# Performance work log

Hardware: AMD Instinct MI355X
Metric: run time of the kernel (lower is better)

The kernel has to match this reference:

```python
import jax, jax.numpy as jnp
import numpy as np

BN_EPS = 1e-5


def _bn(x, gamma, beta):
    # x: [B, C, L]; training-mode BatchNorm1d: biased stats over (B, L) per channel.
    mu = x.mean(axis=(0, 2), keepdims=True)
    var = x.var(axis=(0, 2), keepdims=True)
    return (x - mu) * jax.lax.rsqrt(var + BN_EPS) * gamma[None, :, None] + beta[None, :, None]


def _sblock(x, g1, be1, w1, bi1, g2, be2, w2, bi2):
    # x: [B, m, n] (n == m). bn1 over channel dim n after transpose.
    t = jnp.swapaxes(x, -2, -1)                      # [B, n, m]
    t = jax.nn.relu(_bn(t, g1, be1))
    t = jnp.einsum('bnm,km->bnk', t, w1) + bi1       # Linear(n,n) on last dim
    t = jnp.swapaxes(t, -2, -1)                      # [B, m, n]
    t = jax.nn.relu(_bn(t, g2, be2))                 # bn2 over channel dim m
    t = jnp.einsum('bmn,kn->bmk', t, w2) + bi2       # Linear(m,m) on last dim
    return t


def _forward(x, bn1_gamma, bn1_beta, w1, b1, bn2_gamma, bn2_beta, w2, b2):
    out = x
    num_blocks = w1.shape[0]
    for l in range(num_blocks):
        out = _sblock(out, bn1_gamma[l], bn1_beta[l], w1[l], b1[l],
                      bn2_gamma[l], bn2_beta[l], w2[l], b2[l])
    n, m = out.shape[-2], out.shape[-1]

    # greedy argmax row/col masking on a detached copy (batch index 0, as in torch)
    oc0 = jax.lax.stop_gradient(out[0])              # [n, m]
    neg_inf = jnp.float32(-jnp.inf)

    def body(line, state):
        oc, visited, mask = state
        idx = jnp.argmax(oc)
        i, j = idx // m, idx % m
        visited = visited.at[i].set(1.0)
        mask = mask.at[:, j].set(1.0 - visited)
        oc = oc.at[:, j].set(neg_inf)
        oc = oc.at[i, :].set(neg_inf)
        return oc, visited, mask

    init = (oc0, jnp.zeros((n,), jnp.float32), jnp.zeros((n, m), jnp.float32))
    _, _, mask = jax.lax.fori_loop(0, n, body, init)

    out = jnp.where(mask.astype(bool)[None], neg_inf, out)
    return jax.nn.softmax(out, axis=-1)


def setup_inputs() -> dict:
    key = jax.random.key(0)
    ks = jax.random.split(key, 9)
    L, n, m = 2, 2048, 2048
    return {
        'x': jax.random.normal(ks[0], (1, m, n), jnp.float32),
        'bn1_gamma': jax.random.uniform(ks[1], (L, n), jnp.float32, 0.5, 1.5),
        'bn1_beta': 0.1 * jax.random.normal(ks[2], (L, n), jnp.float32),
        'w1': 0.02 * jax.random.normal(ks[3], (L, n, n), jnp.float32),
        'b1': 0.02 * jax.random.normal(ks[4], (L, n), jnp.float32),
        'bn2_gamma': jax.random.uniform(ks[5], (L, m), jnp.float32, 0.5, 1.5),
        'bn2_beta': 0.1 * jax.random.normal(ks[6], (L, m), jnp.float32),
        'w2': 0.02 * jax.random.normal(ks[7], (L, m, m), jnp.float32),
        'b2': 0.02 * jax.random.normal(ks[8], (L, m), jnp.float32),
    }


def reference(x, bn1_gamma, bn1_beta, w1, b1, bn2_gamma, bn2_beta, w2, b2):
    return _forward(x, bn1_gamma, bn1_beta, w1, b1, bn2_gamma, bn2_beta, w2, b2)
```

## Files before the change

### kernel.cpp

```cpp
#include <hip/hip_runtime.h>
#include <math.h>

#define NEG_INF (-__builtin_inf())

typedef unsigned long long u64;

constexpr int N = 2048;
constexpr int NCHUNK = 32;
constexpr int RPC = N / NCHUNK;
constexpr int K_LIST = 64;
constexpr int BCAND = 128;
constexpr int CMAX = 256;
constexpr int CTGT = 240;
constexpr int POOL_MIN = 48;

template<typename T> struct Key;
template<> struct Key<float>{
  static __device__ inline u64 pack(float x){
    unsigned u = __float_as_uint(x);
    u = (u & 0x80000000u) ? ~u : (u | 0x80000000u);
    return ((u64)u) << 32;
  }
};

__device__ inline bool kbetter(u64 k, unsigned rc, u64 bk, unsigned brc){
  return (k > bk) || (k == bk && rc < brc);
}

template<typename T>
__global__ __launch_bounds__(256) void colstats_partial(const T* __restrict__ X, double* __restrict__ part){
  int col = blockIdx.x * 256 + threadIdx.x;
  int r0  = blockIdx.y * RPC;
  double s = 0.0, q = 0.0;
  for (int r = r0; r < r0 + RPC; ++r){
    double v = (double)X[(size_t)r * N + col];
    s += v; q += v * v;
  }
  size_t o = (size_t)blockIdx.y * N + col;
  part[o*2+0] = s; part[o*2+1] = q;
}

__global__ __launch_bounds__(256) void colstats_final(const double* __restrict__ part,
    const float* __restrict__ g, const float* __restrict__ be,
    double* __restrict__ A, double* __restrict__ C){
  int col = blockIdx.x * 256 + threadIdx.x;
  double s = 0.0, q = 0.0;
  for (int k = 0; k < NCHUNK; ++k){
    size_t o = (size_t)k * N + col;
    s += part[o*2+0]; q += part[o*2+1];
  }
  double mu  = s / (double)N;
  double var = q / (double)N - mu * mu;
  double inv = 1.0 / sqrt(var + 1e-5);
  double a = (double)g[col] * inv;
  A[col] = a;
  C[col] = (double)be[col] - mu * a;
}

template<typename T>
__global__ __launch_bounds__(256) void rowstats(const T* __restrict__ Z,
    const float* __restrict__ g, const float* __restrict__ be,
    double* __restrict__ A, double* __restrict__ C){
  __shared__ double s1[256], s2[256];
  int r = blockIdx.x, tx = threadIdx.x;
  double s = 0.0, q = 0.0;
  for (int j = tx; j < N; j += 256){
    double v = (double)Z[(size_t)r * N + j];
    s += v; q += v * v;
  }
  s1[tx] = s; s2[tx] = q; __syncthreads();
  for (int st = 128; st; st >>= 1){
    if (tx < st){ s1[tx] += s1[tx + st]; s2[tx] += s2[tx + st]; }
    __syncthreads();
  }
  if (tx == 0){
    double mu  = s1[0] / (double)N;
    double var = s2[0] / (double)N - mu * mu;
    double inv = 1.0 / sqrt(var + 1e-5);
    double a = (double)g[r] * inv;
    A[r] = a;
    C[r] = (double)be[r] - mu * a;
  }
}

template<typename Tin, typename Tout>
__global__ __launch_bounds__(256) void bnrelu_col(const Tin* __restrict__ X,
    const double* __restrict__ A, const double* __restrict__ C, Tout* __restrict__ O){
  int i = blockIdx.x;
  for (int j = threadIdx.x; j < N; j += 256){
    double v = fma((double)X[(size_t)i * N + j], A[j], C[j]);
    O[(size_t)i * N + j] = (Tout)(v > 0.0 ? v : 0.0);
  }
}

template<typename Tin, typename Tout>
__global__ __launch_bounds__(256) void bnrelu_row(const Tin* __restrict__ Z,
    const double* __restrict__ A, const double* __restrict__ C, Tout* __restrict__ O){
  int i = blockIdx.x;
  double a = A[i], c = C[i];
  for (int j = threadIdx.x; j < N; j += 256){
    double v = fma((double)Z[(size_t)i * N + j], a, c);
    O[(size_t)i * N + j] = (Tout)(v > 0.0 ? v : 0.0);
  }
}

template<typename TA, typename TB, typename TO, typename TACC, bool BT, bool BIAS_ROW>
__global__ __launch_bounds__(256) void gemm_t(const TA* __restrict__ A, const TB* __restrict__ B,
    const float* __restrict__ bias, TO* __restrict__ O){
  __shared__ TACC sA[16][68];
  __shared__ TACC sB[16][68];
  const int tid = threadIdx.x;
  const int tx = tid & 15, ty = tid >> 4;
  const int i0 = blockIdx.y * 64, j0 = blockIdx.x * 64;
  TACC acc[4][4] = {};
  for (int k0 = 0; k0 < N; k0 += 16){
    {
      int r = tid >> 2, c4 = (tid & 3) * 4;
      const TA* p = A + (size_t)(i0 + r) * N + k0 + c4;
      TACC v0 = (TACC)p[0], v1 = (TACC)p[1], v2 = (TACC)p[2], v3 = (TACC)p[3];
      sA[c4+0][r] = v0; sA[c4+1][r] = v1; sA[c4+2][r] = v2; sA[c4+3][r] = v3;
    }
    if (!BT){
      int k = tid >> 4, j4 = (tid & 15) * 4;
      const TB* p = B + (size_t)(k0 + k) * N + j0 + j4;
      sB[k][j4+0] = (TACC)p[0]; sB[k][j4+1] = (TACC)p[1];
      sB[k][j4+2] = (TACC)p[2]; sB[k][j4+3] = (TACC)p[3];
    } else {
      int j = tid >> 2, c4 = (tid & 3) * 4;
      const TB* p = B + (size_t)(j0 + j) * N + k0 + c4;
      TACC v0 = (TACC)p[0], v1 = (TACC)p[1], v2 = (TACC)p[2], v3 = (TACC)p[3];
      sB[c4+0][j] = v0; sB[c4+1][j] = v1; sB[c4+2][j] = v2; sB[c4+3][j] = v3;
    }
    __syncthreads();
    #pragma unroll
    for (int kk = 0; kk < 16; ++kk){
      TACC a_[4], b_[4];
      #pragma unroll
      for (int q = 0; q < 4; ++q){ a_[q] = sA[kk][ty*4+q]; b_[q] = sB[kk][tx*4+q]; }
      #pragma unroll
      for (int mi = 0; mi < 4; ++mi)
        #pragma unroll
        for (int ni = 0; ni < 4; ++ni)
          acc[mi][ni] = fma(a_[mi], b_[ni], acc[mi][ni]);
    }
    __syncthreads();
  }
  #pragma unroll
  for (int mi = 0; mi < 4; ++mi){
    int i = i0 + ty*4 + mi;
    #pragma unroll
    for (int ni = 0; ni < 4; ++ni){
      int j = j0 + tx*4 + ni;
      TACC bv = BIAS_ROW ? (TACC)bias[i] : (TACC)bias[j];
      O[(size_t)i * N + j] = (TO)(acc[mi][ni] + bv);
    }
  }
}

template<typename T>
__global__ __launch_bounds__(256) void build_lists(const T* __restrict__ O,
    ulonglong2* __restrict__ list, unsigned short* __restrict__ llen,
    u64* __restrict__ rvK_g, unsigned* __restrict__ rvRC_g,
    unsigned* __restrict__ flag){
  __shared__ unsigned hist4[4][256];
  __shared__ unsigned hsum[256];
  __shared__ u64 candK[BCAND];
  __shared__ unsigned candRC[BCAND];
  __shared__ u64 redK[256];
  __shared__ unsigned redC[256];
  __shared__ u64 sTau;
  __shared__ unsigned sBstar, sPre, sDone, sC;
  const int r = blockIdx.x;
  const int tid = threadIdx.x;
  const int wave = tid >> 6, lane = tid & 63;
  const unsigned BIG = 0xFFFFFFFFu;
  const T* __restrict__ row = O + (size_t)r * N;
  const unsigned target = K_LIST;

  if (r == 0 && tid == 0) *flag = 0u;

  u64 base = 0; unsigned pre = 0; int shift = 56;
  for (int level = 0; level < 8; ++level){
    for (int i = tid; i < 4*256; i += 256) ((unsigned*)hist4)[i] = 0;
    __syncthreads();
    for (int c = tid; c < N; c += 256){
      u64 k = Key<T>::pack(row[c]);
      if (k >= base && ((k - base) >> shift) < 256)
        atomicAdd(&hist4[wave][(unsigned)((k - base) >> shift)], 1u);
    }
    __syncthreads();
    if (tid < 256) hsum[tid] = hist4[0][tid] + hist4[1][tid] + hist4[2][tid] + hist4[3][tid];
    __syncthreads();
    if (wave == 0){
      unsigned v0 = hsum[4*lane+0], v1 = hsum[4*lane+1], v2 = hsum[4*lane+2], v3 = hsum[4*lane+3];
      unsigned s3 = v3, s2 = v2+v3, s1 = v1+s2, tot = v0+s1;
      unsigned run = tot;
      #pragma unroll
      for (int off = 1; off < 64; off <<= 1){
        unsigned x = __shfl_down(run, off);
        if (lane + off < 64) run += x;
      }
      unsigned above = run - tot;
      unsigned ge0 = tot + above, ge1 = s1 + above, ge2 = s2 + above, ge3 = s3 + above;
      int bl = -1; unsigned geb = 0, vb = 0;
      if (pre + ge3 >= target){ bl = 4*lane+3; geb = ge3; vb = v3; }
      else if (pre + ge2 >= target){ bl = 4*lane+2; geb = ge2; vb = v2; }
      else if (pre + ge1 >= target){ bl = 4*lane+1; geb = ge1; vb = v1; }
      else if (pre + ge0 >= target){ bl = 4*lane+0; geb = ge0; vb = v0; }
      int bmax = bl;
      #pragma unroll
      for (int off = 32; off; off >>= 1){
        int o = __shfl_xor(bmax, off);
        if (o > bmax) bmax = o;
      }
      if (bmax < 0){
        if (lane == 0){ sBstar = 0; sPre = pre; sDone = 1; }
      } else if (bl == bmax){
        unsigned total = pre + geb;
        sBstar = (unsigned)bmax; sPre = pre + geb - vb;
        sDone = (total <= BCAND || shift == 0) ? 1u : 0u;
      }
    }
    __syncthreads();
    unsigned bstar = sBstar;
    if (sDone){
      if (tid == 0) sTau = base + ((u64)bstar << shift);
      break;
    }
    base += ((u64)bstar << shift);
    pre = sPre;
    shift -= 8;
    __syncthreads();
  }
  __syncthreads();
  const u64 tau = sTau;

  if (tid == 0) sC = 0;
  __syncthreads();
  for (int c = tid; c < N; c += 256){
    u64 k = Key<T>::pack(row[c]);
    if (k >= tau){
      unsigned p = atomicAdd(&sC, 1u);
      if (p < BCAND){ candK[p] = k; candRC[p] = ((unsigned)r << 11) | (unsigned)c; }
    }
  }
  __syncthreads();
  unsigned C = sC;

  if (C > BCAND){
    u64 bk = 0; unsigned bc = BIG;
    for (int c = tid; c < N; c += 256){
      u64 k = Key<T>::pack(row[c]);
      if (k > bk){ bk = k; bc = (unsigned)c; }
    }
    redK[tid] = bk; redC[tid] = bc; __syncthreads();
    for (int st = 128; st; st >>= 1){
      if (tid < st && kbetter(redK[tid+st], redC[tid+st], redK[tid], redC[tid])){
        redK[tid] = redK[tid+st]; redC[tid] = redC[tid+st];
      }
      __syncthreads();
    }
    if (tid == 0){
      llen[r] = 0;
      rvK_g[r] = redK[0];
      rvRC_g[r] = ((unsigned)r << 11) | (redC[0] & 2047u);
    }
    return;
  }

  unsigned S = 64; while (S < C) S <<= 1;
  for (unsigned p = C + tid; p < S; p += 256){ candK[p] = 0; candRC[p] = BIG; }
  __syncthreads();
  for (unsigned k2 = 2; k2 <= S; k2 <<= 1){
    for (unsigned jj = k2 >> 1; jj > 0; jj >>= 1){
      if (tid < (int)(S >> 1)){
        unsigned i = (((unsigned)tid & ~(jj - 1)) << 1) | ((unsigned)tid & (jj - 1));
        unsigned l = i | jj;
        bool up = ((i & k2) == 0);
        u64 ki = candK[i], kl = candK[l];
        unsigned ri = candRC[i], rl = candRC[l];
        bool lBeforeI = (kl > ki) || (kl == ki && rl < ri);
        bool iBeforeL = (ki > kl) || (ki == kl && ri < rl);
        if (up ? lBeforeI : iBeforeL){
          candK[i] = kl; candK[l] = ki; candRC[i] = rl; candRC[l] = ri;
        }
      }
      __syncthreads();
    }
  }

  unsigned outLen = (C < (unsigned)K_LIST) ? C : (unsigned)K_LIST;
  if (tid < (int)outLen){
    ulonglong2 e; e.x = candK[tid]; e.y = (u64)candRC[tid];
    list[(size_t)r * K_LIST + tid] = e;
  }
  if (tid == 0){
    llen[r] = (unsigned short)outLen;
    rvK_g[r] = candK[0];
    rvRC_g[r] = candRC[0];
  }
}

template<typename T>
__global__ __launch_bounds__(512) void greedy9c(const T* __restrict__ O,
    const ulonglong2* __restrict__ list, const unsigned short* __restrict__ llen_g,
    const u64* __restrict__ rvK_g, const unsigned* __restrict__ rvRC_g,
    unsigned* __restrict__ rowStep_g, unsigned* __restrict__ colStep_g,
    unsigned* __restrict__ flag){
  __shared__ u64 rvK[N];
  __shared__ unsigned rvRC[N];
  __shared__ unsigned cm32[N/32];
  __shared__ unsigned short hIdx[N];
  __shared__ unsigned short hLen[N];
  __shared__ unsigned rowStepL[N];
  __shared__ unsigned colStepL[N];
  __shared__ unsigned hist[8][256];
  __shared__ unsigned hsum[256];
  __shared__ u64 candK[CMAX];
  __shared__ unsigned candRC[CMAX];
  __shared__ u64 sortK[CMAX];
  __shared__ unsigned sortRC[CMAX];
  __shared__ unsigned foc[N];
  __shared__ u64 redK8[8];
  __shared__ unsigned redC8[8];
  __shared__ u64 sTau, sTauP;
  __shared__ unsigned sBstar, sPre, sDone, sC, sCnt, sL, sPC;
  const int tid  = threadIdx.x;
  const int lane = tid & 63, wave = tid >> 6;
  const unsigned BIG = 0xFFFFFFFFu;
  const u64 lmask = ((u64)1 << lane) - 1;

  if (blockIdx.x != 0){
    __shared__ unsigned sdone;
    float a = 1.0f;
    const float b = 1.0000001f, c = 1e-7f;
    for (;;){
      if (tid == 0) sdone = atomicAdd(flag, 0u);
      __syncthreads();
      unsigned d = sdone;
      __syncthreads();
      if (d) break;
      #pragma unroll 8
      for (int i = 0; i < 512; ++i) a = fmaf(a, b, c);
      asm volatile("" : "+v"(a));
    }
    return;
  }

  for (int i = tid; i < N; i += 512){
    rvK[i] = rvK_g[i]; rvRC[i] = rvRC_g[i];
    unsigned short L0 = llen_g[i];
    hLen[i] = L0;
    hIdx[i] = (L0 == 0) ? (unsigned short)0xFFFFu : (unsigned short)1;
  }
  if (tid < N/32) cm32[tid] = 0xFFFFFFFFu;
  if (tid == 0){ sPC = 0; sTauP = 0; sCnt = 0; sL = BIG; }
  __syncthreads();

  unsigned t = 0;
  for (int rd = 0; rd < N && t < N; ++rd){
    const unsigned alive = N - t;
    const unsigned PCin = sPC;
    const bool needRadix = (PCin < (unsigned)POOL_MIN) && (PCin < alive);

    unsigned PC;
    u64 tau;
    bool overflow = false;

    if (needRadix){
      const unsigned target = (alive < (unsigned)CTGT) ? alive : (unsigned)CTGT;
      u64 base = 0; unsigned pre = 0; int shift = 56;
      for (int level = 0; level < 8; ++level){
        for (int i = tid; i < 8*256; i += 512) ((unsigned*)hist)[i] = 0;
        __syncthreads();
        #pragma unroll
        for (int rep = 0; rep < 4; ++rep){
          u64 k = rvK[rep*512 + tid];
          if (k >= base && k && ((k - base) >> shift) < 256)
            atomicAdd(&hist[wave][(unsigned)((k - base) >> shift)], 1u);
        }
        __syncthreads();
        if (tid < 256){
          unsigned s = 0;
          #pragma unroll
          for (int w = 0; w < 8; ++w) s += hist[w][tid];
          hsum[tid] = s;
        }
        __syncthreads();
        if (wave == 0){
          unsigned v0 = hsum[4*lane+0], v1 = hsum[4*lane+1], v2 = hsum[4*lane+2], v3 = hsum[4*lane+3];
          unsigned s3 = v3, s2 = v2+v3, s1 = v1+s2, tot = v0+s1;
          unsigned run = tot;
          #pragma unroll
          for (int off = 1; off < 64; off <<= 1){
            unsigned x = __shfl_down(run, off);
            if (lane + off < 64) run += x;
          }
          unsigned above = run - tot;
          unsigned ge0 = tot + above, ge1 = s1 + above, ge2 = s2 + above, ge3 = s3 + above;
          int bl = -1; unsigned geb = 0, vb = 0;
          if (pre + ge3 >= target){ bl = 4*lane+3; geb = ge3; vb = v3; }
          else if (pre + ge2 >= target){ bl = 4*lane+2; geb = ge2; vb = v2; }
          else if (pre + ge1 >= target){ bl = 4*lane+1; geb = ge1; vb = v1; }
          else if (pre + ge0 >= target){ bl = 4*lane+0; geb = ge0; vb = v0; }
          int bmax = bl;
          #pragma unroll
          for (int off = 32; off; off >>= 1){
            int o = __shfl_xor(bmax, off);
            if (o > bmax) bmax = o;
          }
          if (bmax < 0){
            if (lane == 0){ sBstar = 0; sPre = pre; sDone = 1; }
          } else if (bl == bmax){
            unsigned total = pre + geb;
            sBstar = (unsigned)bmax; sPre = pre + geb - vb;
            sDone = (total <= CMAX || shift == 0) ? 1u : 0u;
          }
        }
        __syncthreads();
        unsigned bstar = sBstar;
        if (sDone){
          if (tid == 0){ sTau = base + ((u64)bstar << shift); sC = 0; }
          break;
        }
        base += ((u64)bstar << shift);
        pre = sPre;
        shift -= 8;
        __syncthreads();
      }
      __syncthreads();
      tau = sTau;

      #pragma unroll
      for (int rep = 0; rep < 4; ++rep){
        int i = rep*512 + tid;
        u64 k = rvK[i];
        bool p = (k != 0) && (k >= tau);
        u64 m = __ballot(p);
        unsigned b = 0;
        if (lane == 0) b = atomicAdd(&sC, (unsigned)__popcll(m));
        b = __shfl(b, 0);
        if (p){
          unsigned pos = b + (unsigned)__popcll(m & lmask);
          if (pos < (unsigned)CMAX){ candK[pos] = k; candRC[pos] = rvRC[i]; }
        }
      }
      __syncthreads();
      PC = sC;
      if (tid == 0) sTauP = tau;
      overflow = (PC > (unsigned)CMAX);
    } else {
      PC = PCin;
      tau = sTauP;
    }

    unsigned L;
    if (overflow){
      u64 bk = 0; unsigned brc = BIG;
      for (int i = tid; i < N; i += 512){
        u64 k = rvK[i];
        if (k && kbetter(k, rvRC[i], bk, brc)){ bk = k; brc = rvRC[i]; }
      }
      #pragma unroll
      for (int off = 32; off; off >>= 1){
        u64 ok = __shfl_xor(bk, off);
        unsigned oc = __shfl_xor(brc, off);
        if (kbetter(ok, oc, bk, brc)){ bk = ok; brc = oc; }
      }
      if (lane == 0){ redK8[wave] = bk; redC8[wave] = brc; }
      __syncthreads();
      if (tid == 0){
        u64 fk = redK8[0]; unsigned fc = redC8[0];
        for (int w = 1; w < 8; ++w)
          if (kbetter(redK8[w], redC8[w], fk, fc)){ fk = redK8[w]; fc = redC8[w]; }
        sortK[0] = fk; sortRC[0] = fc;
      }
      __syncthreads();
      L = 1;
    } else {
      if (tid < (int)PC){
        u64 mk = candK[tid]; unsigned mrc = candRC[tid];
        unsigned rank = 0;
        for (unsigned j = 0; j < PC; ++j)
          if (kbetter(candK[j], candRC[j], mk, mrc)) ++rank;
        sortK[rank] = mk; sortRC[rank] = mrc;
      }
      __syncthreads();
      if (tid < (int)PC) foc[sortRC[tid] & 2047u] = BIG;
      __syncthreads();
      if (tid < (int)PC) atomicMin(&foc[sortRC[tid] & 2047u], (unsigned)tid);
      __syncthreads();
      if (tid < (int)PC && foc[sortRC[tid] & 2047u] < (unsigned)tid)
        atomicMin(&sL, (unsigned)tid);
      __syncthreads();
      L = (sL < PC) ? sL : PC;
    }

    if (tid < (int)L){
      unsigned rc = sortRC[tid];
      unsigned r = rc >> 11, c = rc & 2047u;
      rowStepL[r] = t + (unsigned)tid;
      colStepL[c] = t + (unsigned)tid;
      rvK[r] = 0;
      atomicAnd(&cm32[c >> 5], ~(1u << (c & 31)));
    }
    __syncthreads();
    t += L;
    if (t >= N) break;

    #pragma unroll
    for (int rep = 0; rep < 4; ++rep){
      int rr = rep*512 + tid;
      u64 k = rvK[rr];
      if (k == 0) continue;
      unsigned cc = rvRC[rr] & 2047u;
      if ((cm32[cc >> 5] >> (cc & 31)) & 1u) continue;
      unsigned hi = hIdx[rr];
      u64 nk = 0; unsigned nrc = 0;
      if (hi != 0xFFFFu){
        unsigned ln = hLen[rr];
        while (hi < ln){
          ulonglong2 e = list[(size_t)rr * K_LIST + hi];
          ++hi;
          unsigned ec = ((unsigned)e.y) & 2047u;
          if ((cm32[ec >> 5] >> (ec & 31)) & 1u){ nk = e.x; nrc = (unsigned)e.y; break; }
        }
      }
      if (nk){
        rvK[rr] = nk; rvRC[rr] = nrc; hIdx[rr] = (unsigned short)hi;
      } else {
        hIdx[rr] = (unsigned short)0xFFFFu;
        foc[atomicAdd(&sCnt, 1u)] = (unsigned)rr;
      }
    }
    __syncthreads();

    {
      const unsigned cnt = sCnt;
      for (unsigned q = (unsigned)wave; q < cnt; q += 8){
        unsigned rr = foc[q];
        const T* __restrict__ rowp = O + (size_t)rr * N;
        u64 bk = 0; unsigned bc = BIG;
        #pragma unroll
        for (int it = 0; it < N/64; ++it){
          int cc = lane + it*64;
          u64 kk = Key<T>::pack(rowp[cc]);
          if (!((cm32[cc >> 5] >> (cc & 31)) & 1u)) kk = 0;
          if (kbetter(kk, (unsigned)cc, bk, bc)){ bk = kk; bc = (unsigned)cc; }
        }
        #pragma unroll
        for (int off = 32; off; off >>= 1){
          u64 ok = __shfl_xor(bk, off);
          unsigned oc = __shfl_xor(bc, off);
          if (kbetter(ok, oc, bk, bc)){ bk = ok; bc = oc; }
        }
        if (lane == 0){ rvK[rr] = bk; rvRC[rr] = (rr << 11) | (bc & 2047u); }
      }
    }
    __syncthreads();

    if (!overflow){
      if (tid == 0) sC = 0;
      __syncthreads();
      unsigned p = L + (unsigned)tid;
      u64 k = 0; unsigned rr = 0;
      bool keep = false;
      if (p < PC){
        rr = sortRC[p] >> 11;
        k = rvK[rr];
        keep = (k != 0) && (k >= tau);
      }
      u64 m = __ballot(keep);
      unsigned b = 0;
      if (lane == 0) b = atomicAdd(&sC, (unsigned)__popcll(m));
      b = __shfl(b, 0);
      if (keep){
        unsigned pos = b + (unsigned)__popcll(m & lmask);
        candK[pos] = k; candRC[pos] = rvRC[rr];
      }
      __syncthreads();
      if (tid == 0){ sPC = sC; sCnt = 0; sL = BIG; }
    } else {
      if (tid == 0){ sPC = 0; sCnt = 0; sL = BIG; }
    }
    __syncthreads();
  }

  __syncthreads();
  for (int i = tid; i < N; i += 512){
    rowStep_g[i] = rowStepL[i];
    colStep_g[i] = colStepL[i];
  }
  __threadfence();
  if (tid == 0) atomicExch(flag, 1u);
}

template<typename T>
__global__ __launch_bounds__(256) void masked_softmax(const T* __restrict__ O,
    const unsigned* __restrict__ rowStep, const unsigned* __restrict__ colStep,
    float* __restrict__ out){
  __shared__ double vals[N];
  __shared__ double red[256];
  int r = blockIdx.x, tx = threadIdx.x;
  unsigned s = rowStep[r];
  double mx = NEG_INF;
  for (int c = tx; c < N; c += 256){
    double v = (colStep[c] >= s) ? (double)O[(size_t)r * N + c] : NEG_INF;
    vals[c] = v;
    if (v > mx) mx = v;
  }
  red[tx] = mx; __syncthreads();
  for (int st = 128; st; st >>= 1){
    if (tx < st) red[tx] = fmax(red[tx], red[tx + st]);
    __syncthreads();
  }
  mx = red[0]; __syncthreads();
  double sm = 0.0;
  for (int c = tx; c < N; c += 256){
    double v = vals[c];
    double e = (v != NEG_INF) ? exp(v - mx) : 0.0;
    vals[c] = e;
    sm += e;
  }
  red[tx] = sm; __syncthreads();
  for (int st = 128; st; st >>= 1){
    if (tx < st) red[tx] += red[tx + st];
    __syncthreads();
  }
  double inv = 1.0 / red[0];
  for (int c = tx; c < N; c += 256){
    out[(size_t)r * N + c] = (float)(vals[c] * inv);
  }
}

template<typename T>
static void run_pipeline(const float* x, const float* g1, const float* be1,
                         const float* W1, const float* bi1,
                         const float* g2, const float* be2,
                         const float* W2, const float* bi2,
                         float* out, T* buf0, T* buf1,
                         double* part, double* stA, double* stC,
                         u64* rvK, unsigned* rvRC,
                         unsigned* rowStep, unsigned* colStep,
                         ulonglong2* list, unsigned short* llen,
                         unsigned* flag,
                         hipStream_t s){
  dim3 gs(N/256, NCHUNK);
  dim3 gg(N/64, N/64);
  colstats_partial<float><<<gs,256,0,s>>>(x, part);
  colstats_final<<<N/256,256,0,s>>>(part, g1, be1, stA, stC);
  bnrelu_col<float,T><<<N,256,0,s>>>(x, stA, stC, buf0);
  gemm_t<float,T,T,T,false,true><<<gg,256,0,s>>>(W1, buf0, bi1, buf1);
  rowstats<T><<<N,256,0,s>>>(buf1, g2, be2, stA, stC);
  bnrelu_row<T,T><<<N,256,0,s>>>(buf1, stA, stC, buf0);
  gemm_t<T,float,T,T,true,false><<<gg,256,0,s>>>(buf0, W2, bi2, buf1);
  colstats_partial<T><<<gs,256,0,s>>>(buf1, part);
  colstats_final<<<N/256,256,0,s>>>(part, g1+N, be1+N, stA, stC);
  bnrelu_col<T,T><<<N,256,0,s>>>(buf1, stA, stC, buf0);
  gemm_t<float,T,T,T,false,true><<<gg,256,0,s>>>(W1+(size_t)N*N, buf0, bi1+N, buf1);
  rowstats<T><<<N,256,0,s>>>(buf1, g2+N, be2+N, stA, stC);
  bnrelu_row<T,T><<<N,256,0,s>>>(buf1, stA, stC, buf0);
  gemm_t<T,float,T,T,true,false><<<gg,256,0,s>>>(buf0, W2+(size_t)N*N, bi2+N, buf1);
  build_lists<T><<<N,256,0,s>>>(buf1, list, llen, rvK, rvRC, flag);
  greedy9c<T><<<256,512,0,s>>>(buf1, list, llen, rvK, rvRC, rowStep, colStep, flag);
  masked_softmax<T><<<N,256,0,s>>>(buf1, rowStep, colStep, out);
}

extern "C" void kernel_launch(void* const* d_in, const int* in_sizes, int n_in,
                              void* d_out, int out_size, void* d_ws, size_t ws_size,
                              hipStream_t stream){
  if (n_in < 9) return;
  const float* x   = (const float*)d_in[0];
  const float* g1  = (const float*)d_in[1];
  const float* be1 = (const float*)d_in[2];
  const float* W1  = (const float*)d_in[3];
  const float* bi1 = (const float*)d_in[4];
  const float* g2  = (const float*)d_in[5];
  const float* be2 = (const float*)d_in[6];
  const float* W2  = (const float*)d_in[7];
  const float* bi2 = (const float*)d_in[8];
  float* out = (float*)d_out;

  char* base = (char*)d_ws;
  size_t off = 0;
  auto carve = [&](size_t bytes)->void*{
    void* q = base + off;
    off = (off + bytes + 255) & ~(size_t)255;
    return q;
  };
  double*   part    = (double*)carve((size_t)NCHUNK * N * 2 * sizeof(double));
  double*   stA     = (double*)carve(N * sizeof(double));
  double*   stC     = (double*)carve(N * sizeof(double));
  u64*      rvK     = (u64*)carve(N * sizeof(u64));
  unsigned* rvRC    = (unsigned*)carve(N * sizeof(unsigned));
  unsigned* rowStep = (unsigned*)carve(N * sizeof(unsigned));
  unsigned* colStep = (unsigned*)carve(N * sizeof(unsigned));
  ulonglong2* list  = (ulonglong2*)carve((size_t)N * K_LIST * sizeof(ulonglong2));
  unsigned short* llen = (unsigned short*)carve(N * sizeof(unsigned short));
  unsigned* flag    = (unsigned*)carve(256);
  size_t smallEnd = off;

  const size_t matF = (size_t)N * N * sizeof(float);
  size_t needF  = smallEnd + 2 * (matF + 256);
  size_t needF1 = smallEnd + 1 * (matF + 256);

  if (ws_size >= needF){
    float* b0 = (float*)carve(matF);
    float* b1 = (float*)carve(matF);
    run_pipeline<float>(x,g1,be1,W1,bi1,g2,be2,W2,bi2, out, b0, b1,
                        part, stA, stC, rvK, rvRC, rowStep, colStep, list, llen, flag, stream);
  } else if (ws_size >= needF1){
    float* b0 = (float*)carve(matF);
    float* b1 = out;
    run_pipeline<float>(x,g1,be1,W1,bi1,g2,be2,W2,bi2, out, b0, b1,
                        part, stA, stC, rvK, rvRC, rowStep, colStep, list, llen, flag, stream);
  }
}
```

Before: 4.479 ms.

## Replace pooled greedy rounds with event-driven sorted candidate processing and pending heap

The greedy argmax-masking kernel drops the cross-round candidate pool. Each round now re-runs the radix threshold selection, sorts the candidates, and walks them in an event loop. The loop commits runs of valid prefix entries in parallel and handles conflicts serially on thread 0, using per-row fallback lists and a small pending buffer for rows whose next best is still above the threshold. The aim is to commit many more assignments per round and so cut the number of expensive rounds, at the cost of a serial single-thread section, many block barriers per event, and more complex control flow.

```diff
diff --git a/kernel.cpp b/kernel.cpp
--- a/kernel.cpp
+++ b/kernel.cpp
@@ -12,7 +12,7 @@
 constexpr int BCAND = 128;
 constexpr int CMAX = 256;
 constexpr int CTGT = 240;
-constexpr int POOL_MIN = 48;
+constexpr int PMAX = 24;
 
 template<typename T> struct Key;
 template<> struct Key<float>{
@@ -302,7 +302,7 @@
 }
 
 template<typename T>
-__global__ __launch_bounds__(512) void greedy9c(const T* __restrict__ O,
+__global__ __launch_bounds__(512) void greedy11(const T* __restrict__ O,
     const ulonglong2* __restrict__ list, const unsigned short* __restrict__ llen_g,
     const u64* __restrict__ rvK_g, const unsigned* __restrict__ rvRC_g,
     unsigned* __restrict__ rowStep_g, unsigned* __restrict__ colStep_g,
@@ -320,11 +320,15 @@
   __shared__ unsigned candRC[CMAX];
   __shared__ u64 sortK[CMAX];
   __shared__ unsigned sortRC[CMAX];
+  __shared__ unsigned char dupF[CMAX];
   __shared__ unsigned foc[N];
+  __shared__ u64 pK[PMAX];
+  __shared__ unsigned pRC[PMAX];
   __shared__ u64 redK8[8];
   __shared__ unsigned redC8[8];
-  __shared__ u64 sTau, sTauP;
-  __shared__ unsigned sBstar, sPre, sDone, sC, sCnt, sL, sPC;
+  __shared__ u64 sTau, sPMK;
+  __shared__ unsigned sBstar, sPre, sDone, sC, sCnt;
+  __shared__ unsigned sPMRC, sPCnt, sCur, sTl, sD, sBreak, sResc;
   const int tid  = threadIdx.x;
   const int lane = tid & 63, wave = tid >> 6;
   const unsigned BIG = 0xFFFFFFFFu;
@@ -337,9 +341,9 @@
     for (;;){
       if (tid == 0) sdone = atomicAdd(flag, 0u);
       __syncthreads();
-      unsigned d = sdone;
-      __syncthreads();
-      if (d) break;
+      unsigned dd = sdone;
+      __syncthreads();
+      if (dd) break;
       #pragma unroll 8
       for (int i = 0; i < 512; ++i) a = fmaf(a, b, c);
       asm volatile("" : "+v"(a));
@@ -354,108 +358,95 @@
     hIdx[i] = (L0 == 0) ? (unsigned short)0xFFFFu : (unsigned short)1;
   }
   if (tid < N/32) cm32[tid] = 0xFFFFFFFFu;
-  if (tid == 0){ sPC = 0; sTauP = 0; sCnt = 0; sL = BIG; }
+  if (tid == 0){ sCnt = 0; }
   __syncthreads();
 
   unsigned t = 0;
   for (int rd = 0; rd < N && t < N; ++rd){
     const unsigned alive = N - t;
-    const unsigned PCin = sPC;
-    const bool needRadix = (PCin < (unsigned)POOL_MIN) && (PCin < alive);
-
-    unsigned PC;
-    u64 tau;
-    bool overflow = false;
-
-    if (needRadix){
-      const unsigned target = (alive < (unsigned)CTGT) ? alive : (unsigned)CTGT;
-      u64 base = 0; unsigned pre = 0; int shift = 56;
-      for (int level = 0; level < 8; ++level){
-        for (int i = tid; i < 8*256; i += 512) ((unsigned*)hist)[i] = 0;
-        __syncthreads();
-        #pragma unroll
-        for (int rep = 0; rep < 4; ++rep){
-          u64 k = rvK[rep*512 + tid];
-          if (k >= base && k && ((k - base) >> shift) < 256)
-            atomicAdd(&hist[wave][(unsigned)((k - base) >> shift)], 1u);
-        }
-        __syncthreads();
-        if (tid < 256){
-          unsigned s = 0;
-          #pragma unroll
-          for (int w = 0; w < 8; ++w) s += hist[w][tid];
-          hsum[tid] = s;
-        }
-        __syncthreads();
-        if (wave == 0){
-          unsigned v0 = hsum[4*lane+0], v1 = hsum[4*lane+1], v2 = hsum[4*lane+2], v3 = hsum[4*lane+3];
-          unsigned s3 = v3, s2 = v2+v3, s1 = v1+s2, tot = v0+s1;
-          unsigned run = tot;
-          #pragma unroll
-          for (int off = 1; off < 64; off <<= 1){
-            unsigned x = __shfl_down(run, off);
-            if (lane + off < 64) run += x;
-          }
-          unsigned above = run - tot;
-          unsigned ge0 = tot + above, ge1 = s1 + above, ge2 = s2 + above, ge3 = s3 + above;
-          int bl = -1; unsigned geb = 0, vb = 0;
-          if (pre + ge3 >= target){ bl = 4*lane+3; geb = ge3; vb = v3; }
-          else if (pre + ge2 >= target){ bl = 4*lane+2; geb = ge2; vb = v2; }
-          else if (pre + ge1 >= target){ bl = 4*lane+1; geb = ge1; vb = v1; }
-          else if (pre + ge0 >= target){ bl = 4*lane+0; geb = ge0; vb = v0; }
-          int bmax = bl;
-          #pragma unroll
-          for (int off = 32; off; off >>= 1){
-            int o = __shfl_xor(bmax, off);
-            if (o > bmax) bmax = o;
-          }
-          if (bmax < 0){
-            if (lane == 0){ sBstar = 0; sPre = pre; sDone = 1; }
-          } else if (bl == bmax){
-            unsigned total = pre + geb;
-            sBstar = (unsigned)bmax; sPre = pre + geb - vb;
-            sDone = (total <= CMAX || shift == 0) ? 1u : 0u;
-          }
-        }
-        __syncthreads();
-        unsigned bstar = sBstar;
-        if (sDone){
-          if (tid == 0){ sTau = base + ((u64)bstar << shift); sC = 0; }
-          break;
-        }
-        base += ((u64)bstar << shift);
-        pre = sPre;
-        shift -= 8;
-        __syncthreads();
-      }
-      __syncthreads();
-      tau = sTau;
-
+    const unsigned target = (alive < (unsigned)CTGT) ? alive : (unsigned)CTGT;
+    if (tid == 0){ sC = 0; }
+
+    u64 base = 0; unsigned pre = 0; int shift = 56;
+    for (int level = 0; level < 8; ++level){
+      for (int i = tid; i < 8*256; i += 512) ((unsigned*)hist)[i] = 0;
+      __syncthreads();
       #pragma unroll
       for (int rep = 0; rep < 4; ++rep){
-        int i = rep*512 + tid;
-        u64 k = rvK[i];
-        bool p = (k != 0) && (k >= tau);
-        u64 m = __ballot(p);
-        unsigned b = 0;
-        if (lane == 0) b = atomicAdd(&sC, (unsigned)__popcll(m));
-        b = __shfl(b, 0);
-        if (p){
-          unsigned pos = b + (unsigned)__popcll(m & lmask);
-          if (pos < (unsigned)CMAX){ candK[pos] = k; candRC[pos] = rvRC[i]; }
-        }
-      }
-      __syncthreads();
-      PC = sC;
-      if (tid == 0) sTauP = tau;
-      overflow = (PC > (unsigned)CMAX);
-    } else {
-      PC = PCin;
-      tau = sTauP;
-    }
-
-    unsigned L;
-    if (overflow){
+        u64 k = rvK[rep*512 + tid];
+        if (k >= base && k && ((k - base) >> shift) < 256)
+          atomicAdd(&hist[wave][(unsigned)((k - base) >> shift)], 1u);
+      }
+      __syncthreads();
+      if (tid < 256){
+        unsigned s = 0;
+        #pragma unroll
+        for (int w = 0; w < 8; ++w) s += hist[w][tid];
+        hsum[tid] = s;
+      }
+      __syncthreads();
+      if (wave == 0){
+        unsigned v0 = hsum[4*lane+0], v1 = hsum[4*lane+1], v2 = hsum[4*lane+2], v3 = hsum[4*lane+3];
+        unsigned s3 = v3, s2 = v2+v3, s1 = v1+s2, tot = v0+s1;
+        unsigned run = tot;
+        #pragma unroll
+        for (int off = 1; off < 64; off <<= 1){
+          unsigned x = __shfl_down(run, off);
+          if (lane + off < 64) run += x;
+        }
+        unsigned above = run - tot;
+        unsigned ge0 = tot + above, ge1 = s1 + above, ge2 = s2 + above, ge3 = s3 + above;
+        int bl = -1; unsigned geb = 0, vb = 0;
+        if (pre + ge3 >= target){ bl = 4*lane+3; geb = ge3; vb = v3; }
+        else if (pre + ge2 >= target){ bl = 4*lane+2; geb = ge2; vb = v2; }
+        else if (pre + ge1 >= target){ bl = 4*lane+1; geb = ge1; vb = v1; }
+        else if (pre + ge0 >= target){ bl = 4*lane+0; geb = ge0; vb = v0; }
+        int bmax = bl;
+        #pragma unroll
+        for (int off = 32; off; off >>= 1){
+          int o = __shfl_xor(bmax, off);
+          if (o > bmax) bmax = o;
+        }
+        if (bmax < 0){
+          if (lane == 0){ sBstar = 0; sPre = pre; sDone = 1; }
+        } else if (bl == bmax){
+          unsigned total = pre + geb;
+          sBstar = (unsigned)bmax; sPre = pre + geb - vb;
+          sDone = (total <= CMAX || shift == 0) ? 1u : 0u;
+        }
+      }
+      __syncthreads();
+      unsigned bstar = sBstar;
+      if (sDone){
+        if (tid == 0) sTau = base + ((u64)bstar << shift);
+        break;
+      }
+      base += ((u64)bstar << shift);
+      pre = sPre;
+      shift -= 8;
+      __syncthreads();
+    }
+    __syncthreads();
+    const u64 tau = sTau;
+
+    #pragma unroll
+    for (int rep = 0; rep < 4; ++rep){
+      int i = rep*512 + tid;
+      u64 k = rvK[i];
+      bool p = (k != 0) && (k >= tau);
+      u64 m = __ballot(p);
+      unsigned b = 0;
+      if (lane == 0) b = atomicAdd(&sC, (unsigned)__popcll(m));
+      b = __shfl(b, 0);
+      if (p){
+        unsigned pos = b + (unsigned)__popcll(m & lmask);
+        if (pos < (unsigned)CMAX){ candK[pos] = k; candRC[pos] = rvRC[i]; }
+      }
+    }
+    __syncthreads();
+    const unsigned PC = sC;
+
+    if (PC > (unsigned)CMAX){
       u64 bk = 0; unsigned brc = BIG;
       for (int i = tid; i < N; i += 512){
         u64 k = rvK[i];
@@ -473,41 +464,190 @@
         u64 fk = redK8[0]; unsigned fc = redC8[0];
         for (int w = 1; w < 8; ++w)
           if (kbetter(redK8[w], redC8[w], fk, fc)){ fk = redK8[w]; fc = redC8[w]; }
-        sortK[0] = fk; sortRC[0] = fc;
-      }
-      __syncthreads();
-      L = 1;
+        unsigned r = fc >> 11, c = fc & 2047u;
+        rowStepL[r] = t; colStepL[c] = t;
+        rvK[r] = 0;
+        cm32[c >> 5] &= ~(1u << (c & 31));
+        sTl = t + 1;
+      }
+      __syncthreads();
+      t = sTl;
     } else {
       if (tid < (int)PC){
         u64 mk = candK[tid]; unsigned mrc = candRC[tid];
         unsigned rank = 0;
+        #pragma unroll 4
         for (unsigned j = 0; j < PC; ++j)
           if (kbetter(candK[j], candRC[j], mk, mrc)) ++rank;
         sortK[rank] = mk; sortRC[rank] = mrc;
       }
       __syncthreads();
+
       if (tid < (int)PC) foc[sortRC[tid] & 2047u] = BIG;
       __syncthreads();
       if (tid < (int)PC) atomicMin(&foc[sortRC[tid] & 2047u], (unsigned)tid);
       __syncthreads();
-      if (tid < (int)PC && foc[sortRC[tid] & 2047u] < (unsigned)tid)
-        atomicMin(&sL, (unsigned)tid);
-      __syncthreads();
-      L = (sL < PC) ? sL : PC;
-    }
-
-    if (tid < (int)L){
-      unsigned rc = sortRC[tid];
-      unsigned r = rc >> 11, c = rc & 2047u;
-      rowStepL[r] = t + (unsigned)tid;
-      colStepL[c] = t + (unsigned)tid;
-      rvK[r] = 0;
-      atomicAnd(&cm32[c >> 5], ~(1u << (c & 31)));
-    }
-    __syncthreads();
-    t += L;
+      if (tid < (int)PC) dupF[tid] = (foc[sortRC[tid] & 2047u] < (unsigned)tid) ? 1 : 0;
+      if (tid == 0){ sCur = 0; sTl = t; sPCnt = 0; sPMK = 0; sPMRC = BIG; sBreak = 0; sResc = BIG; }
+      __syncthreads();
+
+      for (int ev = 0; ev < 2048; ++ev){
+        if (tid == 0) sD = PC;
+        __syncthreads();
+        {
+          unsigned cur = sCur;
+          unsigned pcnt = sPCnt; u64 pmk = sPMK; unsigned pmrc = sPMRC;
+          if (tid >= (int)cur && tid < (int)PC){
+            unsigned c = sortRC[tid] & 2047u;
+            bool dead = !((cm32[c>>5] >> (c&31)) & 1u);
+            bool pend = (pcnt > 0) && kbetter(pmk, pmrc, sortK[tid], sortRC[tid]);
+            if (dupF[tid] || dead || pend) atomicMin(&sD, (unsigned)tid);
+          }
+        }
+        __syncthreads();
+        const unsigned cur0 = sCur, d = sD, tl0 = sTl;
+        if (tid >= (int)cur0 && tid < (int)d){
+          unsigned rc = sortRC[tid];
+          unsigned r = rc >> 11, c = rc & 2047u;
+          rowStepL[r] = tl0 + ((unsigned)tid - cur0);
+          colStepL[c] = tl0 + ((unsigned)tid - cur0);
+          rvK[r] = 0;
+          atomicAnd(&cm32[c >> 5], ~(1u << (c & 31)));
+        }
+        __syncthreads();
+        if (tid == 0){
+          unsigned cur = d;
+          unsigned tl = tl0 + (d - cur0);
+          unsigned pcnt = sPCnt;
+          sResc = BIG;
+          if (cur >= PC && pcnt == 0){
+            sBreak = 1; sCur = cur; sTl = tl;
+          } else {
+            u64 pmk = 0; unsigned pmrc = BIG, pmi = 0;
+            for (unsigned q = 0; q < pcnt; ++q)
+              if (kbetter(pK[q], pRC[q], pmk, pmrc)){ pmk = pK[q]; pmrc = pRC[q]; pmi = q; }
+            bool pWins = (pcnt > 0) && (cur >= PC || kbetter(pmk, pmrc, sortK[cur], sortRC[cur]));
+            if (pWins){
+              unsigned prr = pmrc >> 11, pcc = pmrc & 2047u;
+              if ((cm32[pcc>>5] >> (pcc&31)) & 1u){
+                rowStepL[prr] = tl; colStepL[pcc] = tl; ++tl;
+                rvK[prr] = 0;
+                cm32[pcc>>5] &= ~(1u << (pcc&31));
+                pK[pmi] = pK[pcnt-1]; pRC[pmi] = pRC[pcnt-1]; --pcnt;
+              } else {
+                u64 nk = 0; unsigned nrc = BIG;
+                unsigned hi = hIdx[prr];
+                if (hi != 0xFFFFu){
+                  unsigned ln = hLen[prr];
+                  while (hi < ln){
+                    ulonglong2 e = list[(size_t)prr * K_LIST + hi]; ++hi;
+                    unsigned ec = (unsigned)e.y & 2047u;
+                    if ((cm32[ec>>5] >> (ec&31)) & 1u){ nk = e.x; nrc = (unsigned)e.y; break; }
+                  }
+                  if (!nk) hi = 0xFFFFu;
+                  hIdx[prr] = (unsigned short)hi;
+                }
+                if (nk){
+                  if (nk >= tau){ pK[pmi] = nk; pRC[pmi] = nrc; }
+                  else { rvK[prr] = nk; rvRC[prr] = nrc;
+                         pK[pmi] = pK[pcnt-1]; pRC[pmi] = pRC[pcnt-1]; --pcnt; }
+                } else {
+                  sResc = prr;
+                  pK[pmi] = pK[pcnt-1]; pRC[pmi] = pRC[pcnt-1]; --pcnt;
+                }
+              }
+            } else {
+              unsigned rc = sortRC[cur];
+              unsigned rr = rc >> 11, cc = rc & 2047u;
+              if ((cm32[cc>>5] >> (cc&31)) & 1u){
+                rowStepL[rr] = tl; colStepL[cc] = tl; ++tl;
+                rvK[rr] = 0;
+                cm32[cc>>5] &= ~(1u << (cc&31));
+              } else {
+                u64 nk = 0; unsigned nrc = BIG;
+                unsigned hi = hIdx[rr];
+                if (hi != 0xFFFFu){
+                  unsigned ln = hLen[rr];
+                  while (hi < ln){
+                    ulonglong2 e = list[(size_t)rr * K_LIST + hi]; ++hi;
+                    unsigned ec = (unsigned)e.y & 2047u;
+                    if ((cm32[ec>>5] >> (ec&31)) & 1u){ nk = e.x; nrc = (unsigned)e.y; break; }
+                  }
+                  if (!nk) hi = 0xFFFFu;
+                  hIdx[rr] = (unsigned short)hi;
+                }
+                if (nk){
+                  if (nk >= tau){
+                    if (pcnt < (unsigned)PMAX){ pK[pcnt] = nk; pRC[pcnt] = nrc; ++pcnt; }
+                    else { rvK[rr] = nk; rvRC[rr] = nrc; sBreak = 1; }
+                  } else { rvK[rr] = nk; rvRC[rr] = nrc; }
+                } else {
+                  sResc = rr;
+                }
+              }
+              ++cur;
+            }
+            sCur = cur; sTl = tl; sPCnt = pcnt;
+            u64 mk = 0; unsigned mrc = BIG;
+            for (unsigned q = 0; q < pcnt; ++q)
+              if (kbetter(pK[q], pRC[q], mk, mrc)){ mk = pK[q]; mrc = pRC[q]; }
+            sPMK = mk; sPMRC = mrc;
+          }
+        }
+        __syncthreads();
+        if (sBreak) break;
+        if (sResc != BIG){
+          unsigned rr = sResc;
+          const T* __restrict__ rowp = O + (size_t)rr * N;
+          u64 bk = 0; unsigned bc = BIG;
+          for (int cc = tid; cc < N; cc += 512){
+            u64 kk = Key<T>::pack(rowp[cc]);
+            if (!((cm32[cc>>5] >> (cc&31)) & 1u)) kk = 0;
+            if (kbetter(kk, (unsigned)cc, bk, bc)){ bk = kk; bc = (unsigned)cc; }
+          }
+          #pragma unroll
+          for (int off = 32; off; off >>= 1){
+            u64 ok = __shfl_xor(bk, off);
+            unsigned oc = __shfl_xor(bc, off);
+            if (kbetter(ok, oc, bk, bc)){ bk = ok; bc = oc; }
+          }
+          if (lane == 0){ redK8[wave] = bk; redC8[wave] = bc; }
+          __syncthreads();
+          if (tid == 0){
+            u64 fk = redK8[0]; unsigned fc = redC8[0];
+            for (int w = 1; w < 8; ++w)
+              if (kbetter(redK8[w], redC8[w], fk, fc)){ fk = redK8[w]; fc = redC8[w]; }
+            unsigned nrc = (rr << 11) | (fc & 2047u);
+            unsigned pcnt = sPCnt;
+            hIdx[rr] = (unsigned short)0xFFFFu;
+            if (fk && fk >= tau){
+              if (pcnt < (unsigned)PMAX){
+                pK[pcnt] = fk; pRC[pcnt] = nrc; sPCnt = pcnt + 1;
+                if (kbetter(fk, nrc, sPMK, sPMRC)){ sPMK = fk; sPMRC = nrc; }
+              } else { rvK[rr] = fk; rvRC[rr] = nrc; sBreak = 1; }
+            } else { rvK[rr] = fk; rvRC[rr] = nrc; }
+            sResc = BIG;
+          }
+          __syncthreads();
+          if (sBreak) break;
+        }
+      }
+
+      {
+        unsigned pcnt = sPCnt;
+        if (tid < (int)pcnt){
+          unsigned rc = pRC[tid];
+          rvK[rc >> 11] = pK[tid];
+          rvRC[rc >> 11] = rc;
+        }
+      }
+      __syncthreads();
+      t = sTl;
+    }
     if (t >= N) break;
 
+    if (tid == 0) sCnt = 0;
+    __syncthreads();
     #pragma unroll
     for (int rep = 0; rep < 4; ++rep){
       int rr = rep*512 + tid;
@@ -556,32 +696,6 @@
         }
         if (lane == 0){ rvK[rr] = bk; rvRC[rr] = (rr << 11) | (bc & 2047u); }
       }
-    }
-    __syncthreads();
-
-    if (!overflow){
-      if (tid == 0) sC = 0;
-      __syncthreads();
-      unsigned p = L + (unsigned)tid;
-      u64 k = 0; unsigned rr = 0;
-      bool keep = false;
-      if (p < PC){
-        rr = sortRC[p] >> 11;
-        k = rvK[rr];
-        keep = (k != 0) && (k >= tau);
-      }
-      u64 m = __ballot(keep);
-      unsigned b = 0;
-      if (lane == 0) b = atomicAdd(&sC, (unsigned)__popcll(m));
-      b = __shfl(b, 0);
-      if (keep){
-        unsigned pos = b + (unsigned)__popcll(m & lmask);
-        candK[pos] = k; candRC[pos] = rvRC[rr];
-      }
-      __syncthreads();
-      if (tid == 0){ sPC = sC; sCnt = 0; sL = BIG; }
-    } else {
-      if (tid == 0){ sPC = 0; sCnt = 0; sL = BIG; }
     }
     __syncthreads();
   }
@@ -662,7 +776,7 @@
   bnrelu_row<T,T><<<N,256,0,s>>>(buf1, stA, stC, buf0);
   gemm_t<T,float,T,T,true,false><<<gg,256,0,s>>>(buf0, W2+(size_t)N*N, bi2+N, buf1);
   build_lists<T><<<N,256,0,s>>>(buf1, list, llen, rvK, rvRC, flag);
-  greedy9c<T><<<256,512,0,s>>>(buf1, list, llen, rvK, rvRC, rowStep, colStep, flag);
+  greedy11<T><<<256,512,0,s>>>(buf1, list, llen, rvK, rvRC, rowStep, colStep, flag);
   masked_softmax<T><<<N,256,0,s>>>(buf1, rowStep, colStep, out);
 }
 
```

After: 7.987 ms. +78.3%, slower.
